# Optimization experiments

Measured on AMD Instinct MI355X. Metric: run time of the kernel, lower is better.

Reference implementation:

```python
import jax, jax.numpy as jnp
import numpy as np

NUM_HEADS = 16


def setup_inputs() -> dict:
    key = jax.random.key(0)
    k1, k2, k3, k4 = jax.random.split(key, 4)
    B, S, E = 2, 2048, 1024
    x = jax.random.normal(k1, (B, S, E), dtype=jnp.float32)
    src_padding_mask = jax.random.randint(k2, (B, S), 0, 2) > 0  # True = keep
    # xavier-uniform-ish scale for linear weights (shape (out, in), torch convention)
    w_qkv = jax.random.normal(k3, (3 * E, E), dtype=jnp.float32) * (1.0 / np.sqrt(E))
    w_o = jax.random.normal(k4, (E, E), dtype=jnp.float32) * (1.0 / np.sqrt(E))
    return {"x": x, "src_padding_mask": src_padding_mask, "w_qkv": w_qkv, "w_o": w_o}


def reference(x, src_padding_mask, w_qkv, w_o):
    B, S, E = x.shape
    H = NUM_HEADS
    D = E // H
    # fused qkv projection: (B,S,3E) -> (B,S,H,3D) -> split
    qkv = jnp.einsum("bse,fe->bsf", x, w_qkv).reshape(B, S, H, 3 * D)
    q, k, v = jnp.split(qkv, 3, axis=-1)
    # (B,H,S,D)
    q = q.transpose(0, 2, 1, 3)
    k = k.transpose(0, 2, 1, 3)
    v = v.transpose(0, 2, 1, 3)
    logits = jnp.einsum("bhqd,bhkd->bhqk", q, k) / jnp.sqrt(jnp.float32(D))
    logits = jnp.where(src_padding_mask[:, None, None, :], logits, -jnp.inf)
    attn = jax.nn.softmax(logits, axis=-1)
    values = jnp.einsum("bhqk,bhkd->bhqd", attn, v)  # (B,H,S,D)
    values = values.transpose(0, 2, 1, 3).reshape(B, S, E)
    out = jnp.einsum("bse,fe->bsf", values, w_o)
    return out
```

## Files before the change

### kernel.cpp

```cpp
#include <hip/hip_runtime.h>
#include <hip/hip_bf16.h>

#define B_NUM 2
#define S_LEN 2048
#define E_DIM 1024
#define H_NUM 16
#define D_DIM 64
#define QKV_LD 3072

typedef __attribute__((ext_vector_type(8))) short bf16x8;
typedef __attribute__((ext_vector_type(8))) unsigned short u16x8;
typedef __attribute__((ext_vector_type(4))) unsigned short u16x4;
typedef __attribute__((ext_vector_type(4))) float f32x4;
typedef __attribute__((ext_vector_type(16))) float f32x16;
typedef __attribute__((ext_vector_type(2))) int i32x2;

static __device__ __forceinline__ unsigned short f2bf(float f) {
    union { float f; unsigned int u; } v; v.f = f;
    unsigned int r = v.u + 0x7fffu + ((v.u >> 16) & 1u);
    return (unsigned short)(r >> 16);
}

static __device__ __forceinline__ unsigned cvtpk_bf16(float lo, float hi) {
    unsigned r;
    asm("v_cvt_pk_bf16_f32 %0, %1, %2" : "=v"(r) : "v"(lo), "v"(hi));
    return r;
}

__global__ __launch_bounds__(256)
void cvt_f32_bf16(const float* __restrict__ in, unsigned short* __restrict__ outp, int n4) {
    int i = blockIdx.x * blockDim.x + threadIdx.x;
    if (i < n4) {
        float4 f = ((const float4*)in)[i];
        u16x4 o = { f2bf(f.x), f2bf(f.y), f2bf(f.z), f2bf(f.w) };
        ((u16x4*)outp)[i] = o;
    }
}

template <bool OUT_BF16, bool QSCALE>
__global__ __launch_bounds__(256)
void gemm_bt_mfma(const unsigned short* __restrict__ A,
                  const unsigned short* __restrict__ Bw,
                  void* __restrict__ Cv, int M, int N, int K) {
    __shared__ unsigned short As[64 * 64];
    __shared__ unsigned short Bs[64 * 64];
    char* const AsB = (char*)As;
    char* const BsB = (char*)Bs;
    const int tid  = threadIdx.x;
    const int lane = tid & 63;
    const int w    = tid >> 6;
    const int lg   = lane >> 4;
    const int lq   = lane & 15;
    const int bm = blockIdx.y * 64;
    const int bn = blockIdx.x * 64;
    const int wr = (w >> 1) * 32;
    const int wc = (w & 1) * 32;
    const int sr = tid >> 2;
    const int sc = (tid & 3) * 16;
    const int swzS = (sr & 7) << 4;

    f32x4 acc[2][2];
#pragma unroll
    for (int i = 0; i < 2; ++i)
#pragma unroll
        for (int j = 0; j < 2; ++j) acc[i][j] = (f32x4){0.f, 0.f, 0.f, 0.f};

    const unsigned short* ap = A  + (size_t)(bm + sr) * K + sc;
    const unsigned short* bp = Bw + (size_t)(bn + sr) * K + sc;

    for (int k0 = 0; k0 < K; k0 += 64) {
        __syncthreads();
        u16x8 av0 = *(const u16x8*)(ap + k0);
        u16x8 av1 = *(const u16x8*)(ap + k0 + 8);
        u16x8 bv0 = *(const u16x8*)(bp + k0);
        u16x8 bv1 = *(const u16x8*)(bp + k0 + 8);
        *(u16x8*)(AsB + sr * 128 + ((sc * 2)      ^ swzS)) = av0;
        *(u16x8*)(AsB + sr * 128 + ((sc * 2 + 16) ^ swzS)) = av1;
        *(u16x8*)(BsB + sr * 128 + ((sc * 2)      ^ swzS)) = bv0;
        *(u16x8*)(BsB + sr * 128 + ((sc * 2 + 16) ^ swzS)) = bv1;
        __syncthreads();

        bf16x8 af[2][2], bfr[2][2];
#pragma unroll
        for (int rt = 0; rt < 2; ++rt) {
            const int row = wr + rt * 16 + lq;
            const int sz = (row & 7) << 4;
            af[rt][0] = *(const bf16x8*)(AsB + row * 128 + ((lg * 16)      ^ sz));
            af[rt][1] = *(const bf16x8*)(AsB + row * 128 + ((64 + lg * 16) ^ sz));
        }
#pragma unroll
        for (int ct = 0; ct < 2; ++ct) {
            const int row = wc + ct * 16 + lq;
            const int sz = (row & 7) << 4;
            bfr[ct][0] = *(const bf16x8*)(BsB + row * 128 + ((lg * 16)      ^ sz));
            bfr[ct][1] = *(const bf16x8*)(BsB + row * 128 + ((64 + lg * 16) ^ sz));
        }
#pragma unroll
        for (int rt = 0; rt < 2; ++rt)
#pragma unroll
            for (int ct = 0; ct < 2; ++ct) {
                acc[rt][ct] = __builtin_amdgcn_mfma_f32_16x16x32_bf16(af[rt][0], bfr[ct][0], acc[rt][ct], 0, 0, 0);
                acc[rt][ct] = __builtin_amdgcn_mfma_f32_16x16x32_bf16(af[rt][1], bfr[ct][1], acc[rt][ct], 0, 0, 0);
            }
    }

#pragma unroll
    for (int rt = 0; rt < 2; ++rt)
#pragma unroll
        for (int ct = 0; ct < 2; ++ct) {
            const int row = bm + wr + rt * 16 + lg * 4;
            const int col = bn + wc + ct * 16 + lq;
            float scale = 1.f;
            if constexpr (QSCALE) scale = ((col % 192) < 64) ? 0.125f : 1.f;
#pragma unroll
            for (int r = 0; r < 4; ++r) {
                float vv = acc[rt][ct][r] * scale;
                if constexpr (OUT_BF16)
                    ((unsigned short*)Cv)[(size_t)(row + r) * N + col] = f2bf(vv);
                else
                    ((float*)Cv)[(size_t)(row + r) * N + col] = vv;
            }
        }
}

__global__ __launch_bounds__(256)
void attn_mfma32(const unsigned short* __restrict__ qkv, const int* __restrict__ mask,
                 unsigned short* __restrict__ vout) {
    __shared__ unsigned short Ks[64 * 64];
    __shared__ unsigned short Vt[64 * 64];
    __shared__ __align__(16) float MskF[64];
    char* const KsB = (char*)Ks;
    char* const VtB = (char*)Vt;

    const int tid  = threadIdx.x;
    const int lane = tid & 63;
    const int w    = tid >> 6;
    const int ln   = lane & 31;
    const int hi   = lane >> 5;
    const int q0 = blockIdx.x * 128;
    const int h  = blockIdx.y;
    const int b  = blockIdx.z;
    const size_t baseBH = (size_t)b * S_LEN * QKV_LD + (size_t)h * (3 * D_DIM);

    bf16x8 qf[4];
    {
        const unsigned short* qp = qkv + baseBH + (size_t)(q0 + w * 32 + ln) * QKV_LD + hi * 8;
#pragma unroll
        for (int kk = 0; kk < 4; ++kk)
            qf[kk] = *(const bf16x8*)(qp + kk * 16);
    }

    f32x16 accO[2];
#pragma unroll
    for (int dt = 0; dt < 2; ++dt)
#pragma unroll
        for (int r = 0; r < 16; ++r) accO[dt][r] = 0.f;
    float mrun = 0.f, lrow = 0.f;

    const int ksr = tid >> 2;
    const int ksc = (tid & 3) * 16;
    const int vkb = (tid & 15) * 4;
    const int vdb = (tid >> 4) * 4;

    for (int kv0 = 0; kv0 < S_LEN; kv0 += 64) {
        __syncthreads();
        {
            const unsigned short* kp = qkv + baseBH + (size_t)(kv0 + ksr) * QKV_LD + D_DIM + ksc;
            u16x8 a0 = *(const u16x8*)kp;
            u16x8 a1 = *(const u16x8*)(kp + 8);
            const int swz = (ksr & 7) << 4;
            *(u16x8*)(KsB + ksr * 128 + ((ksc * 2)      ^ swz)) = a0;
            *(u16x8*)(KsB + ksr * 128 + ((ksc * 2 + 16) ^ swz)) = a1;
        }
        {
            u16x4 vr[4];
#pragma unroll
            for (int i = 0; i < 4; ++i)
                vr[i] = *(const u16x4*)(qkv + baseBH + (size_t)(kv0 + vkb + i) * QKV_LD + 2 * D_DIM + vdb);
#pragma unroll
            for (int j = 0; j < 4; ++j) {
                u16x4 o = { vr[0][j], vr[1][j], vr[2][j], vr[3][j] };
                const int row = vdb + j;
                *(u16x4*)(VtB + row * 128 + ((vkb * 2) ^ ((row & 7) << 4))) = o;
            }
        }
        if (tid < 64) MskF[tid] = (mask[b * S_LEN + kv0 + tid] != 0) ? 0.f : -30000.f;
        __syncthreads();

        f32x16 s[2];
#pragma unroll
        for (int ks = 0; ks < 2; ++ks)
#pragma unroll
            for (int m = 0; m < 4; ++m) {
                f32x4 b4 = *(const f32x4*)(MskF + ks * 32 + m * 8 + hi * 4);
#pragma unroll
                for (int i = 0; i < 4; ++i) s[ks][m * 4 + i] = b4[i];
            }
#pragma unroll
        for (int ks = 0; ks < 2; ++ks) {
            const int krow = ks * 32 + ln;
            const int swz = (ln & 7) << 4;
#pragma unroll
            for (int kk = 0; kk < 4; ++kk) {
                bf16x8 kf = *(const bf16x8*)(KsB + krow * 128 + (((kk * 16 + hi * 8) * 2) ^ swz));
                s[ks] = __builtin_amdgcn_mfma_f32_32x32x16_bf16(kf, qf[kk], s[ks], 0, 0, 0);
            }
        }

        float tm = -3.4e38f;
#pragma unroll
        for (int ks = 0; ks < 2; ++ks)
#pragma unroll
            for (int r = 0; r < 16; ++r) tm = fmaxf(tm, s[ks][r]);
        {
            i32x2 rr = __builtin_amdgcn_permlane32_swap(__float_as_int(tm), __float_as_int(tm), false, false);
            tm = fmaxf(__int_as_float(rr[0]), __int_as_float(rr[1]));
        }
        const float mnew = fmaxf(mrun, tm);
        const float fsc = __expf(mrun - mnew);
        mrun = mnew;
        float rsum = 0.f;
#pragma unroll
        for (int ks = 0; ks < 2; ++ks)
#pragma unroll
            for (int r = 0; r < 16; ++r) {
                float p = __expf(s[ks][r] - mnew);
                s[ks][r] = p;
                rsum += p;
            }
        {
            i32x2 rr = __builtin_amdgcn_permlane32_swap(__float_as_int(rsum), __float_as_int(rsum), false, false);
            rsum = __int_as_float(rr[0]) + __int_as_float(rr[1]);
        }
        lrow = lrow * fsc + rsum;
#pragma unroll
        for (int dt = 0; dt < 2; ++dt)
#pragma unroll
            for (int r = 0; r < 16; ++r) accO[dt][r] *= fsc;

        bf16x8 pb[4];
#pragma unroll
        for (int ks = 0; ks < 2; ++ks) {
            unsigned wA[4], wB[4];
#pragma unroll
            for (int m = 0; m < 4; ++m) {
                wA[m] = cvtpk_bf16(s[ks][4 * m + 0], s[ks][4 * m + 1]);
                wB[m] = cvtpk_bf16(s[ks][4 * m + 2], s[ks][4 * m + 3]);
            }
#pragma unroll
            for (int t = 0; t < 2; ++t) {
                i32x2 ra = __builtin_amdgcn_permlane32_swap((int)wA[2 * t], (int)wA[2 * t + 1], false, false);
                i32x2 rb = __builtin_amdgcn_permlane32_swap((int)wB[2 * t], (int)wB[2 * t + 1], false, false);
                union { unsigned u[4]; bf16x8 v; } uu;
                uu.u[0] = (unsigned)ra[0];
                uu.u[1] = (unsigned)rb[0];
                uu.u[2] = (unsigned)ra[1];
                uu.u[3] = (unsigned)rb[1];
                pb[ks * 2 + t] = uu.v;
            }
        }

#pragma unroll
        for (int dt = 0; dt < 2; ++dt) {
            const int drow = dt * 32 + ln;
            const int swz = (ln & 7) << 4;
#pragma unroll
            for (int n = 0; n < 4; ++n) {
                bf16x8 va = *(const bf16x8*)(VtB + drow * 128 + (((n * 16 + hi * 8) * 2) ^ swz));
                accO[dt] = __builtin_amdgcn_mfma_f32_32x32x16_bf16(va, pb[n], accO[dt], 0, 0, 0);
            }
        }
    }

    const float inv = 1.f / lrow;
    unsigned short* op = vout + (size_t)(b * S_LEN + q0 + w * 32 + ln) * E_DIM + h * D_DIM;
#pragma unroll
    for (int dt = 0; dt < 2; ++dt)
#pragma unroll
        for (int m = 0; m < 4; ++m) {
            u16x4 o;
#pragma unroll
            for (int i = 0; i < 4; ++i) o[i] = f2bf(accO[dt][4 * m + i] * inv);
            *(u16x4*)(op + dt * 32 + m * 8 + hi * 4) = o;
        }
}

extern "C" void kernel_launch(void* const* d_in, const int* in_sizes, int n_in,
                              void* d_out, int out_size, void* d_ws, size_t ws_size,
                              hipStream_t stream) {
    const float* x      = (const float*)d_in[0];
    const int*   mask   = (const int*)d_in[1];
    const float* w_qkv  = (const float*)d_in[2];
    const float* w_o    = (const float*)d_in[3];
    float*       out    = (float*)d_out;

    const int M = B_NUM * S_LEN;
    unsigned short* qkvb = (unsigned short*)d_ws;
    unsigned short* vbuf = qkvb + (size_t)M * 3 * E_DIM;
    unsigned short* xb   = vbuf + (size_t)M * E_DIM;
    unsigned short* wqb  = xb   + (size_t)M * E_DIM;
    unsigned short* wob  = wqb  + (size_t)3 * E_DIM * E_DIM;

    dim3 blk(256);
    {
        int n4;
        n4 = M * E_DIM / 4;
        cvt_f32_bf16<<<dim3((n4 + 255) / 256), blk, 0, stream>>>(x, xb, n4);
        n4 = 3 * E_DIM * E_DIM / 4;
        cvt_f32_bf16<<<dim3((n4 + 255) / 256), blk, 0, stream>>>(w_qkv, wqb, n4);
        n4 = E_DIM * E_DIM / 4;
        cvt_f32_bf16<<<dim3((n4 + 255) / 256), blk, 0, stream>>>(w_o, wob, n4);
    }

    gemm_bt_mfma<true, true><<<dim3(3 * E_DIM / 64, M / 64), blk, 0, stream>>>(
        xb, wqb, qkvb, M, 3 * E_DIM, E_DIM);

    attn_mfma32<<<dim3(S_LEN / 128, H_NUM, B_NUM), blk, 0, stream>>>(qkvb, mask, vbuf);

    gemm_bt_mfma<false, false><<<dim3(E_DIM / 64, M / 64), blk, 0, stream>>>(
        vbuf, wob, out, M, E_DIM, E_DIM);
}
```

Measured before the change: 149.7 us.

## Use 128x128 LDS-DMA GEMM for QKV and split-KV attention with lazy rescale

Adds a 128x128-tile GEMM for the QKV projection that loads its A and B tiles straight into LDS through global_load_lds with an XOR swizzle, raising reuse per block. The attention kernel moves to 512 threads, and two groups of four waves each handle half the key sequence. The halves are merged at the end through LDS using their running max and sum. It also skips the softmax rescale whenever the new tile max stays within 8 of the running max. Together these aim to cut global traffic, increase parallelism within each block, and remove exp/multiply work, at the cost of higher LDS and register pressure and a final merge step.

```diff
diff --git a/kernel.cpp b/kernel.cpp
--- a/kernel.cpp
+++ b/kernel.cpp
@@ -25,6 +25,12 @@
     unsigned r;
     asm("v_cvt_pk_bf16_f32 %0, %1, %2" : "=v"(r) : "v"(lo), "v"(hi));
     return r;
+}
+
+static __device__ __forceinline__ void gload16(const void* gsrc, void* ldst) {
+    __builtin_amdgcn_global_load_lds(
+        (const __attribute__((address_space(1))) unsigned int*)gsrc,
+        (__attribute__((address_space(3))) unsigned int*)ldst, 16, 0, 0);
 }
 
 __global__ __launch_bounds__(256)
@@ -35,6 +41,87 @@
         u16x4 o = { f2bf(f.x), f2bf(f.y), f2bf(f.z), f2bf(f.w) };
         ((u16x4*)outp)[i] = o;
     }
+}
+
+template <bool OUT_BF16, bool QSCALE>
+__global__ __launch_bounds__(256)
+void gemm_bt_mfma128(const unsigned short* __restrict__ A,
+                     const unsigned short* __restrict__ Bw,
+                     void* __restrict__ Cv, int M, int N, int K) {
+    __shared__ unsigned short As[128 * 64];
+    __shared__ unsigned short Bs[128 * 64];
+    char* const AsB = (char*)As;
+    char* const BsB = (char*)Bs;
+    const int tid  = threadIdx.x;
+    const int lane = tid & 63;
+    const int w    = tid >> 6;
+    const int lg   = lane >> 4;
+    const int lq   = lane & 15;
+    const int bm = blockIdx.y * 128;
+    const int bn = blockIdx.x * 128;
+    const int wr = (w >> 1) * 64;
+    const int wc = (w & 1) * 64;
+    const int lrow8 = lane >> 3;
+    const int gblk  = (lane & 7) ^ lrow8;
+
+    f32x4 acc[4][4];
+#pragma unroll
+    for (int i = 0; i < 4; ++i)
+#pragma unroll
+        for (int j = 0; j < 4; ++j) acc[i][j] = (f32x4){0.f, 0.f, 0.f, 0.f};
+
+    for (int k0 = 0; k0 < K; k0 += 64) {
+        __syncthreads();
+#pragma unroll
+        for (int t = 0; t < 4; ++t) {
+            const int c = w * 4 + t;
+            const int row = c * 8 + lrow8;
+            gload16(A + (size_t)(bm + row) * K + k0 + gblk * 8, AsB + c * 1024);
+            gload16(Bw + (size_t)(bn + row) * K + k0 + gblk * 8, BsB + c * 1024);
+        }
+        __syncthreads();
+
+        bf16x8 af[4][2], bfr[4][2];
+#pragma unroll
+        for (int rt = 0; rt < 4; ++rt) {
+            const int row = wr + rt * 16 + lq;
+            const int sz = (row & 7) << 4;
+            af[rt][0] = *(const bf16x8*)(AsB + row * 128 + ((lg * 16)      ^ sz));
+            af[rt][1] = *(const bf16x8*)(AsB + row * 128 + ((64 + lg * 16) ^ sz));
+        }
+#pragma unroll
+        for (int ct = 0; ct < 4; ++ct) {
+            const int row = wc + ct * 16 + lq;
+            const int sz = (row & 7) << 4;
+            bfr[ct][0] = *(const bf16x8*)(BsB + row * 128 + ((lg * 16)      ^ sz));
+            bfr[ct][1] = *(const bf16x8*)(BsB + row * 128 + ((64 + lg * 16) ^ sz));
+        }
+#pragma unroll
+        for (int rt = 0; rt < 4; ++rt)
+#pragma unroll
+            for (int ct = 0; ct < 4; ++ct) {
+                acc[rt][ct] = __builtin_amdgcn_mfma_f32_16x16x32_bf16(af[rt][0], bfr[ct][0], acc[rt][ct], 0, 0, 0);
+                acc[rt][ct] = __builtin_amdgcn_mfma_f32_16x16x32_bf16(af[rt][1], bfr[ct][1], acc[rt][ct], 0, 0, 0);
+            }
+    }
+
+#pragma unroll
+    for (int rt = 0; rt < 4; ++rt)
+#pragma unroll
+        for (int ct = 0; ct < 4; ++ct) {
+            const int row = bm + wr + rt * 16 + lg * 4;
+            const int col = bn + wc + ct * 16 + lq;
+            float scale = 1.f;
+            if constexpr (QSCALE) scale = ((col % 192) < 64) ? 0.125f : 1.f;
+#pragma unroll
+            for (int r = 0; r < 4; ++r) {
+                float vv = acc[rt][ct][r] * scale;
+                if constexpr (OUT_BF16)
+                    ((unsigned short*)Cv)[(size_t)(row + r) * N + col] = f2bf(vv);
+                else
+                    ((float*)Cv)[(size_t)(row + r) * N + col] = vv;
+            }
+        }
 }
 
 template <bool OUT_BF16, bool QSCALE>
@@ -123,28 +210,33 @@
         }
 }
 
-__global__ __launch_bounds__(256)
-void attn_mfma32(const unsigned short* __restrict__ qkv, const int* __restrict__ mask,
-                 unsigned short* __restrict__ vout) {
-    __shared__ unsigned short Ks[64 * 64];
-    __shared__ unsigned short Vt[64 * 64];
-    __shared__ __align__(16) float MskF[64];
-    char* const KsB = (char*)Ks;
-    char* const VtB = (char*)Vt;
+__global__ __launch_bounds__(512, 4)
+void attn_mfma32_split(const unsigned short* __restrict__ qkv, const int* __restrict__ mask,
+                       unsigned short* __restrict__ vout) {
+    __shared__ __align__(16) char pool[32768];
+    __shared__ __align__(16) float MskF[2][64];
+    __shared__ float Ml[4][64];
 
     const int tid  = threadIdx.x;
     const int lane = tid & 63;
-    const int w    = tid >> 6;
+    const int wid  = tid >> 6;
+    const int g    = wid >> 2;
+    const int w    = wid & 3;
+    const int tg   = tid & 255;
     const int ln   = lane & 31;
     const int hi   = lane >> 5;
     const int q0 = blockIdx.x * 128;
     const int h  = blockIdx.y;
     const int b  = blockIdx.z;
     const size_t baseBH = (size_t)b * S_LEN * QKV_LD + (size_t)h * (3 * D_DIM);
+    const unsigned short* const kv = qkv + baseBH;
+
+    char* const KsB = pool + g * 8192;
+    char* const VtB = pool + 16384 + g * 8192;
 
     bf16x8 qf[4];
     {
-        const unsigned short* qp = qkv + baseBH + (size_t)(q0 + w * 32 + ln) * QKV_LD + hi * 8;
+        const unsigned short* qp = kv + (size_t)(q0 + w * 32 + ln) * QKV_LD + hi * 8;
 #pragma unroll
         for (int kk = 0; kk < 4; ++kk)
             qf[kk] = *(const bf16x8*)(qp + kk * 16);
@@ -157,26 +249,29 @@
         for (int r = 0; r < 16; ++r) accO[dt][r] = 0.f;
     float mrun = 0.f, lrow = 0.f;
 
-    const int ksr = tid >> 2;
-    const int ksc = (tid & 3) * 16;
-    const int vkb = (tid & 15) * 4;
-    const int vdb = (tid >> 4) * 4;
-
-    for (int kv0 = 0; kv0 < S_LEN; kv0 += 64) {
+    const int lrow8 = lane >> 3;
+    const int gblk  = (lane & 7) ^ lrow8;
+    const int vkb = (tg & 15) * 4;
+    const int vdb = (tg >> 4) * 4;
+
+    const int kvbase = g * 1024;
+    for (int it = 0; it < 16; ++it) {
+        const int kv0 = kvbase + it * 64;
         __syncthreads();
         {
-            const unsigned short* kp = qkv + baseBH + (size_t)(kv0 + ksr) * QKV_LD + D_DIM + ksc;
-            u16x8 a0 = *(const u16x8*)kp;
-            u16x8 a1 = *(const u16x8*)(kp + 8);
-            const int swz = (ksr & 7) << 4;
-            *(u16x8*)(KsB + ksr * 128 + ((ksc * 2)      ^ swz)) = a0;
-            *(u16x8*)(KsB + ksr * 128 + ((ksc * 2 + 16) ^ swz)) = a1;
+#pragma unroll
+            for (int t = 0; t < 2; ++t) {
+                const int c = w * 2 + t;
+                const int row = c * 8 + lrow8;
+                gload16(kv + (size_t)(kv0 + row) * QKV_LD + D_DIM + gblk * 8,
+                        KsB + c * 1024);
+            }
         }
         {
             u16x4 vr[4];
 #pragma unroll
             for (int i = 0; i < 4; ++i)
-                vr[i] = *(const u16x4*)(qkv + baseBH + (size_t)(kv0 + vkb + i) * QKV_LD + 2 * D_DIM + vdb);
+                vr[i] = *(const u16x4*)(kv + (size_t)(kv0 + vkb + i) * QKV_LD + 2 * D_DIM + vdb);
 #pragma unroll
             for (int j = 0; j < 4; ++j) {
                 u16x4 o = { vr[0][j], vr[1][j], vr[2][j], vr[3][j] };
@@ -184,7 +279,7 @@
                 *(u16x4*)(VtB + row * 128 + ((vkb * 2) ^ ((row & 7) << 4))) = o;
             }
         }
-        if (tid < 64) MskF[tid] = (mask[b * S_LEN + kv0 + tid] != 0) ? 0.f : -30000.f;
+        if (tg < 64) MskF[g][tg] = (mask[b * S_LEN + kv0 + tg] != 0) ? 0.f : -30000.f;
         __syncthreads();
 
         f32x16 s[2];
@@ -192,7 +287,7 @@
         for (int ks = 0; ks < 2; ++ks)
 #pragma unroll
             for (int m = 0; m < 4; ++m) {
-                f32x4 b4 = *(const f32x4*)(MskF + ks * 32 + m * 8 + hi * 4);
+                f32x4 b4 = *(const f32x4*)(&MskF[g][ks * 32 + m * 8 + hi * 4]);
 #pragma unroll
                 for (int i = 0; i < 4; ++i) s[ks][m * 4 + i] = b4[i];
             }
@@ -216,27 +311,37 @@
             i32x2 rr = __builtin_amdgcn_permlane32_swap(__float_as_int(tm), __float_as_int(tm), false, false);
             tm = fmaxf(__int_as_float(rr[0]), __int_as_float(rr[1]));
         }
-        const float mnew = fmaxf(mrun, tm);
-        const float fsc = __expf(mrun - mnew);
-        mrun = mnew;
         float rsum = 0.f;
-#pragma unroll
-        for (int ks = 0; ks < 2; ++ks)
-#pragma unroll
-            for (int r = 0; r < 16; ++r) {
-                float p = __expf(s[ks][r] - mnew);
-                s[ks][r] = p;
-                rsum += p;
-            }
-        {
+        if (__all(tm <= mrun + 8.f)) {
+#pragma unroll
+            for (int ks = 0; ks < 2; ++ks)
+#pragma unroll
+                for (int r = 0; r < 16; ++r) {
+                    float p = __expf(s[ks][r] - mrun);
+                    s[ks][r] = p;
+                    rsum += p;
+                }
             i32x2 rr = __builtin_amdgcn_permlane32_swap(__float_as_int(rsum), __float_as_int(rsum), false, false);
-            rsum = __int_as_float(rr[0]) + __int_as_float(rr[1]);
-        }
-        lrow = lrow * fsc + rsum;
-#pragma unroll
-        for (int dt = 0; dt < 2; ++dt)
-#pragma unroll
-            for (int r = 0; r < 16; ++r) accO[dt][r] *= fsc;
+            lrow += __int_as_float(rr[0]) + __int_as_float(rr[1]);
+        } else {
+            const float mnew = fmaxf(mrun, tm);
+            const float fsc = __expf(mrun - mnew);
+#pragma unroll
+            for (int ks = 0; ks < 2; ++ks)
+#pragma unroll
+                for (int r = 0; r < 16; ++r) {
+                    float p = __expf(s[ks][r] - mnew);
+                    s[ks][r] = p;
+                    rsum += p;
+                }
+            i32x2 rr = __builtin_amdgcn_permlane32_swap(__float_as_int(rsum), __float_as_int(rsum), false, false);
+            lrow = lrow * fsc + __int_as_float(rr[0]) + __int_as_float(rr[1]);
+            mrun = mnew;
+#pragma unroll
+            for (int dt = 0; dt < 2; ++dt)
+#pragma unroll
+                for (int r = 0; r < 16; ++r) accO[dt][r] *= fsc;
+        }
 
         bf16x8 pb[4];
 #pragma unroll
@@ -272,17 +377,42 @@
         }
     }
 
-    const float inv = 1.f / lrow;
-    unsigned short* op = vout + (size_t)(b * S_LEN + q0 + w * 32 + ln) * E_DIM + h * D_DIM;
-#pragma unroll
-    for (int dt = 0; dt < 2; ++dt)
-#pragma unroll
-        for (int m = 0; m < 4; ++m) {
-            u16x4 o;
-#pragma unroll
-            for (int i = 0; i < 4; ++i) o[i] = f2bf(accO[dt][4 * m + i] * inv);
-            *(u16x4*)(op + dt * 32 + m * 8 + hi * 4) = o;
-        }
+    __syncthreads();
+    if (g == 1) {
+        float* region = (float*)(pool + w * 8192);
+#pragma unroll
+        for (int dt = 0; dt < 2; ++dt)
+#pragma unroll
+            for (int m = 0; m < 4; ++m)
+#pragma unroll
+                for (int i = 0; i < 4; ++i)
+                    region[(dt * 32 + 8 * m + 4 * hi + i) * 32 + ln] = accO[dt][4 * m + i];
+        if (hi == 0) { Ml[w][ln] = mrun; Ml[w][32 + ln] = lrow; }
+    }
+    __syncthreads();
+    if (g == 0) {
+        const float* region = (const float*)(pool + w * 8192);
+        const float m2 = Ml[w][ln];
+        const float l2 = Ml[w][32 + ln];
+        const float mm = fmaxf(mrun, m2);
+        const float f1 = __expf(mrun - mm);
+        const float f2 = __expf(m2 - mm);
+        const float inv = 1.f / (lrow * f1 + l2 * f2);
+        unsigned short* op = vout + (size_t)(b * S_LEN + q0 + w * 32 + ln) * E_DIM + h * D_DIM;
+#pragma unroll
+        for (int dt = 0; dt < 2; ++dt)
+#pragma unroll
+            for (int m = 0; m < 4; ++m) {
+                u16x4 o;
+#pragma unroll
+                for (int i = 0; i < 4; ++i) {
+                    float vv = accO[dt][4 * m + i] * f1
+                             + region[(dt * 32 + 8 * m + 4 * hi + i) * 32 + ln] * f2;
+                    o[i] = f2bf(vv * inv);
+                }
+                *(u16x4*)(op + dt * 32 + m * 8 + hi * 4) = o;
+            }
+    }
 }
 
 extern "C" void kernel_launch(void* const* d_in, const int* in_sizes, int n_in,
@@ -312,10 +442,11 @@
         cvt_f32_bf16<<<dim3((n4 + 255) / 256), blk, 0, stream>>>(w_o, wob, n4);
     }
 
-    gemm_bt_mfma<true, true><<<dim3(3 * E_DIM / 64, M / 64), blk, 0, stream>>>(
+    gemm_bt_mfma128<true, true><<<dim3(3 * E_DIM / 128, M / 128), blk, 0, stream>>>(
         xb, wqb, qkvb, M, 3 * E_DIM, E_DIM);
 
-    attn_mfma32<<<dim3(S_LEN / 128, H_NUM, B_NUM), blk, 0, stream>>>(qkvb, mask, vbuf);
+    attn_mfma32_split<<<dim3(S_LEN / 128, H_NUM, B_NUM), dim3(512), 0, stream>>>(
+        qkvb, mask, vbuf);
 
     gemm_bt_mfma<false, false><<<dim3(E_DIM / 64, M / 64), blk, 0, stream>>>(
         vbuf, wob, out, M, E_DIM, E_DIM);
```

New measurement: 252.5 us. 68.7% more time.
